# Performance work log

Hardware: AMD Instinct MI355X
Metric: run time of the kernel (lower is better)

## Reference

```python
import jax, jax.numpy as jnp
import numpy as np

B, S, H = 2, 2048, 2048
NH, NKV, HD = 16, 4, 128
NEG = -1e9


def rotate_half(x):
    x1, x2 = x[..., : x.shape[-1] // 2], x[..., x.shape[-1] // 2 :]
    return jnp.concatenate((-x2, x1), axis=-1)


def setup_inputs() -> dict:
    key = jax.random.key(0)
    ks = jax.random.split(key, 6)
    hidden_states = jax.random.normal(ks[0], (B, S, H), dtype=jnp.float32)
    # causal additive mask [B, 1, S, S]
    causal = jnp.tril(jnp.ones((S, S), dtype=bool))
    attention_mask = jnp.where(causal, 0.0, NEG).astype(jnp.float32)
    attention_mask = jnp.broadcast_to(attention_mask, (B, 1, S, S))
    # rotary embeddings, base 10000
    inv_freq = 1.0 / (10000.0 ** (np.arange(0, HD, 2, dtype=np.float32) / HD))
    pos = np.arange(S, dtype=np.float32)
    freqs = np.outer(pos, inv_freq)  # [S, HD/2]
    emb = np.concatenate([freqs, freqs], axis=-1)  # [S, HD]
    cos = jnp.broadcast_to(jnp.asarray(np.cos(emb)), (B, S, HD))
    sin = jnp.broadcast_to(jnp.asarray(np.sin(emb)), (B, S, HD))
    sc = 0.02
    Wq = jax.random.normal(ks[1], (H, NH * HD), dtype=jnp.float32) * sc
    Wk = jax.random.normal(ks[2], (H, NKV * HD), dtype=jnp.float32) * sc
    Wv = jax.random.normal(ks[3], (H, NKV * HD), dtype=jnp.float32) * sc
    Wo = jax.random.normal(ks[4], (H, H), dtype=jnp.float32) * sc
    return {"hidden_states": hidden_states, "attention_mask": attention_mask,
            "cos": cos, "sin": sin, "Wq": Wq, "Wk": Wk, "Wv": Wv, "Wo": Wo}


def reference(hidden_states, attention_mask, cos, sin, Wq, Wk, Wv, Wo):
    b, s, _ = hidden_states.shape
    # projections -> [b, heads, s, hd]
    q = (hidden_states @ Wq).reshape(b, s, NH, HD).transpose(0, 2, 1, 3)
    k = (hidden_states @ Wk).reshape(b, s, NKV, HD).transpose(0, 2, 1, 3)
    v = (hidden_states @ Wv).reshape(b, s, NKV, HD).transpose(0, 2, 1, 3)
    # RoPE (cos/sin unsqueezed at dim 1)
    c, sn = cos[:, None], sin[:, None]
    q = q * c + rotate_half(q) * sn
    k = k * c + rotate_half(k) * sn
    # GQA repeat_kv: [b, nkv, s, hd] -> [b, nh, s, hd]
    n_rep = NH // NKV
    k = jnp.repeat(k, n_rep, axis=1)
    v = jnp.repeat(v, n_rep, axis=1)
    scores = jnp.einsum("bhqd,bhkd->bhqk", q, k) / jnp.sqrt(jnp.float32(HD))
    scores = scores + attention_mask
    probs = jax.nn.softmax(scores.astype(jnp.float32), axis=-1).astype(q.dtype)
    out = jnp.einsum("bhqk,bhkd->bhqd", probs, v)
    out = out.transpose(0, 2, 1, 3).reshape(b, s, NH * HD)
    return out @ Wo
```

## Files before the change

kernel.cpp:

```cpp
#include <hip/hip_runtime.h>
#include <hip/hip_bf16.h>

typedef __bf16 bf16;
typedef __bf16 bf16x4 __attribute__((ext_vector_type(4)));
typedef __bf16 bf16x8 __attribute__((ext_vector_type(8)));
typedef float f32x4 __attribute__((ext_vector_type(4)));

__device__ __forceinline__ void gload_lds16(const void* g, void* l) {
  __builtin_amdgcn_global_load_lds((__attribute__((address_space(1))) void*)(g),
                                   (__attribute__((address_space(3))) void*)(l), 16, 0, 0);
}
__device__ __forceinline__ float fexp2(float x) {
  float r;
  asm volatile("v_exp_f32 %0, %1" : "=v"(r) : "v"(x));
  return r;
}
#define S_WAITCNT_VM(n) asm volatile("s_waitcnt vmcnt(" #n ")" ::: "memory")

__global__ void k_diag(float* __restrict__ o, float v) { o[threadIdx.x] = v; }

__global__ void k_cvt_bf16(const float* __restrict__ x, bf16* __restrict__ y, int n4) {
  int i = blockIdx.x * blockDim.x + threadIdx.x;
  if (i < n4) {
    float4 v = reinterpret_cast<const float4*>(x)[i];
    bf16x4 o = {(bf16)v.x, (bf16)v.y, (bf16)v.z, (bf16)v.w};
    reinterpret_cast<bf16x4*>(y)[i] = o;
  }
}

__global__ void k_transpose_w(const float* __restrict__ W, bf16* __restrict__ Wt, int K, int N) {
  __shared__ float tile[32][33];
  int kb = blockIdx.x * 32, nb = blockIdx.y * 32;
  int tx = threadIdx.x & 31, ty = threadIdx.x >> 5;
#pragma unroll
  for (int i = 0; i < 32; i += 8)
    tile[ty + i][tx] = W[(size_t)(kb + ty + i) * N + nb + tx];
  __syncthreads();
#pragma unroll
  for (int i = 0; i < 32; i += 8)
    Wt[(size_t)(nb + ty + i) * K + kb + tx] = (bf16)tile[tx][ty + i];
}

__global__ void k_transpose_v(const bf16* __restrict__ Cq, bf16* __restrict__ Vt) {
  __shared__ bf16 tile[32][34];
  constexpr int S = 2048, CSTR = 3072;
  int sb = blockIdx.x * 32, db = blockIdx.y * 32, bh = blockIdx.z;
  int b = bh >> 2, kvh = bh & 3;
  int tx = threadIdx.x & 31, ty = threadIdx.x >> 5;
  const bf16* src = Cq + (size_t)b * S * CSTR + 2560 + kvh * 128;
#pragma unroll
  for (int i = 0; i < 32; i += 8)
    tile[ty + i][tx] = src[(size_t)(sb + ty + i) * CSTR + db + tx];
  __syncthreads();
  bf16* dst = Vt + (size_t)bh * 128 * S;
#pragma unroll
  for (int i = 0; i < 32; i += 8)
    dst[(size_t)(db + ty + i) * S + sb + tx] = tile[tx][ty + i];
}

template <typename OT>
__global__ __launch_bounds__(512) void k_gemm3(const bf16* __restrict__ A,
                                               const bf16* __restrict__ B0,
                                               const bf16* __restrict__ B1, int nsplit,
                                               OT* __restrict__ C, int Ncols, int Kd) {
  __shared__ __align__(16) bf16 lds_[65536];
  char* lds = (char*)lds_;
  const int t = threadIdx.x, w = t >> 6, l = t & 63;
  const int lr = l & 15, lk = l >> 4;
  const int gx = gridDim.x;
  const int flat = blockIdx.y * gx + blockIdx.x;
  const int xcd = flat & 7, local = flat >> 3;
  const int mi = (xcd & 3) * (gx >> 2) + (local & ((gx >> 2) - 1));
  const int ni = (xcd >> 2) * (gridDim.y >> 1) + (local >> 2);
  const int m0 = mi * 256, n0 = ni * 256;
  const int wm = w >> 2, wn = w & 3;
  const bf16* Bt = (n0 < nsplit) ? B0 + (size_t)n0 * Kd : B1 + (size_t)(n0 - nsplit) * Kd;
  const int nkt = Kd >> 6;
  const int srow = l >> 2;
  const int lch = (l & 3) ^ ((srow + (srow >> 2)) & 3);
  auto stA = [&](int tile, int unit) {
    if (tile >= nkt) return;
    const bf16* s = A + (size_t)(m0 + unit * 64 + (w >> 1) * 16 + srow) * Kd +
                    (tile << 6) + (w & 1) * 32 + lch * 8;
    gload_lds16(s, lds + (tile & 1) * 32768 + unit * 8192 + w * 1024);
  };
  auto stB = [&](int tile, int grp) {
    if (tile >= nkt) return;
    const bf16* s = Bt + (size_t)((w >> 1) * 64 + grp * 16 + srow) * Kd +
                    (tile << 6) + (w & 1) * 32 + lch * 8;
    gload_lds16(s, lds + 65536 + (tile & 1) * 32768 + grp * 8192 + w * 1024);
  };
  const int rdoff = lr * 64 + ((lk ^ ((lr + (lr >> 2)) & 3)) << 4);

  f32x4 acc[8][4] = {};
  stA(0, 0); stA(0, 1); stA(0, 2); stA(0, 3);
  stB(0, 0);
  stA(1, 0); stB(0, 1); stA(1, 1); stB(0, 2); stA(1, 2); stB(0, 3);

  for (int kt = 0; kt < nkt; ++kt) {
    const int buf = kt & 1;
    const char* Ab = lds + buf * 32768;
    const char* Bb = lds + 65536 + buf * 32768;
    bf16x8 af[8][2];
#pragma unroll
    for (int p = 0; p < 4; ++p) {
      if (kt + 1 < nkt) { S_WAITCNT_VM(6); } else { S_WAITCNT_VM(0); }
      __builtin_amdgcn_sched_barrier(0);
      __builtin_amdgcn_s_barrier();
      __builtin_amdgcn_sched_barrier(0);
      if (p == 0) stA(kt + 1, 3); else stA(kt + 2, p - 1);
      stB(kt + 1, p);
      if (p == 0) {
#pragma unroll
        for (int i = 0; i < 8; ++i) {
          const char* ub = Ab + (wm * 2 + (i >> 2)) * 8192 + (i & 3) * 2048;
          af[i][0] = *reinterpret_cast<const bf16x8*>(ub + rdoff);
          af[i][1] = *reinterpret_cast<const bf16x8*>(ub + 1024 + rdoff);
        }
      }
      bf16x8 b0 = *reinterpret_cast<const bf16x8*>(Bb + p * 8192 + wn * 2048 + rdoff);
      bf16x8 b1 = *reinterpret_cast<const bf16x8*>(Bb + p * 8192 + wn * 2048 + 1024 + rdoff);
      __builtin_amdgcn_s_setprio(1);
#pragma unroll
      for (int i = 0; i < 8; ++i) {
        acc[i][p] = __builtin_amdgcn_mfma_f32_16x16x32_bf16(af[i][0], b0, acc[i][p], 0, 0, 0);
        acc[i][p] = __builtin_amdgcn_mfma_f32_16x16x32_bf16(af[i][1], b1, acc[i][p], 0, 0, 0);
      }
      __builtin_amdgcn_s_setprio(0);
      __builtin_amdgcn_sched_barrier(0);
    }
  }
#pragma unroll
  for (int i = 0; i < 8; ++i)
#pragma unroll
    for (int j = 0; j < 4; ++j)
#pragma unroll
      for (int r = 0; r < 4; ++r) {
        int row = m0 + wm * 128 + i * 16 + lk * 4 + r;
        int col = n0 + wn * 64 + j * 16 + lr;
        if constexpr (sizeof(OT) == 4)
          C[(size_t)row * Ncols + col] = acc[i][j][r];
        else
          C[(size_t)row * Ncols + col] = (bf16)acc[i][j][r];
      }
}

template <int BM, typename OT>
__global__ __launch_bounds__(512) void k_gemm2(const bf16* __restrict__ A, const bf16* __restrict__ Bt,
                                               OT* __restrict__ C, int N, int Kd) {
  constexpr int NA = (BM / 16) * 2;
  constexpr int NB = 16;
  constexpr int NST = NA + NB;
  constexpr int NSW = NST / 8;
  constexpr int WM = BM / 4;
  constexpr int RG = WM / 16;
  __shared__ __align__(16) bf16 sAB[2][NST * 512];
  const int t = threadIdx.x, w = t >> 6, l = t & 63;
  const int lr = l & 15, lk = l >> 4;
  const int gx = gridDim.x;
  const int nwg = gx * gridDim.y;
  const int flat = blockIdx.y * gx + blockIdx.x;
  const int vid = (flat & 7) * (nwg >> 3) + (flat >> 3);
  const int m0 = (vid % gx) * BM, n0 = (vid / gx) * 128;
  const int wm = w >> 1, wn = w & 1;
  const int srow = l >> 2;
  const int lchunk = (l & 3) ^ (((l >> 5) & 1) << 1);
  const int rdoff = lr * 64 + ((lk * 16) ^ ((lr >> 3) << 5));
  const int nkt = Kd >> 6;
  char* lds = (char*)sAB;

  auto stage = [&](int kt, int buf) {
    const int k0 = kt << 6;
#pragma unroll
    for (int u = 0; u < NSW; ++u) {
      const int s = w * NSW + u;
      const bf16* src;
      if (s < NA)
        src = A + (size_t)(m0 + (s >> 1) * 16 + srow) * Kd + k0 + (s & 1) * 32 + lchunk * 8;
      else
        src = Bt + (size_t)(n0 + ((s - NA) >> 1) * 16 + srow) * Kd + k0 + ((s - NA) & 1) * 32 + lchunk * 8;
      gload_lds16(src, lds + buf * (NST * 1024) + s * 1024);
    }
  };

  f32x4 acc[RG][4] = {};
  stage(0, 0);
  stage(1, 1);
  if constexpr (NSW == 6) S_WAITCNT_VM(6); else S_WAITCNT_VM(4);
  __builtin_amdgcn_s_barrier();
  int c = 0;
  for (int kt = 0; kt < nkt; ++kt) {
    __builtin_amdgcn_sched_barrier(0);
    const char* base = lds + c * (NST * 1024);
    bf16x8 af[RG][2], bfr[4][2];
#pragma unroll
    for (int i = 0; i < RG; ++i)
#pragma unroll
      for (int kk = 0; kk < 2; ++kk)
        af[i][kk] = *reinterpret_cast<const bf16x8*>(base + ((wm * RG + i) * 2 + kk) * 1024 + rdoff);
#pragma unroll
    for (int j = 0; j < 4; ++j)
#pragma unroll
      for (int kk = 0; kk < 2; ++kk)
        bfr[j][kk] = *reinterpret_cast<const bf16x8*>(base + (NA + (wn * 4 + j) * 2 + kk) * 1024 + rdoff);
    __builtin_amdgcn_s_setprio(1);
#pragma unroll
    for (int i = 0; i < RG; ++i)
#pragma unroll
      for (int j = 0; j < 4; ++j) {
        acc[i][j] = __builtin_amdgcn_mfma_f32_16x16x32_bf16(af[i][0], bfr[j][0], acc[i][j], 0, 0, 0);
        acc[i][j] = __builtin_amdgcn_mfma_f32_16x16x32_bf16(af[i][1], bfr[j][1], acc[i][j], 0, 0, 0);
      }
    __builtin_amdgcn_s_setprio(0);
    __builtin_amdgcn_sched_barrier(0);
    asm volatile("" ::: "memory");
    __builtin_amdgcn_s_barrier();
    if (kt + 2 < nkt) stage(kt + 2, c);
    if (kt + 1 < nkt) {
      if (kt + 2 < nkt) {
        if constexpr (NSW == 6) S_WAITCNT_VM(6); else S_WAITCNT_VM(4);
      } else {
        S_WAITCNT_VM(0);
      }
      asm volatile("" ::: "memory");
      __builtin_amdgcn_s_barrier();
    }
    c ^= 1;
  }
#pragma unroll
  for (int i = 0; i < RG; ++i)
#pragma unroll
    for (int j = 0; j < 4; ++j)
#pragma unroll
      for (int r = 0; r < 4; ++r) {
        int row = m0 + wm * WM + i * 16 + lk * 4 + r;
        int col = n0 + wn * 64 + j * 16 + lr;
        if constexpr (sizeof(OT) == 4)
          C[(size_t)row * N + col] = acc[i][j][r];
        else
          C[(size_t)row * N + col] = (bf16)acc[i][j][r];
      }
}

__global__ void k_rope(bf16* __restrict__ X, const float* __restrict__ cs, const float* __restrict__ sn,
                       int nh, int rowstride, float scale, int total) {
  int idx = blockIdx.x * blockDim.x + threadIdx.x;
  if (idx >= total) return;
  int d = idx & 63;
  int th = idx >> 6;
  int h = th % nh;
  int tok = th / nh;
  size_t base = (size_t)tok * rowstride + h * 128;
  float c = cs[tok * 128 + d], s = sn[tok * 128 + d];
  float x1 = (float)X[base + d];
  float x2 = (float)X[base + d + 64];
  X[base + d] = (bf16)((x1 * c - x2 * s) * scale);
  X[base + d + 64] = (bf16)((x2 * c + x1 * s) * scale);
}

__global__ __launch_bounds__(256) void k_attn(const bf16* __restrict__ Q, const bf16* __restrict__ KV,
                                              const bf16* __restrict__ Vt, bf16* __restrict__ O) {
  constexpr int S = 2048, HD = 128, QSTR = 3072, OSTR = 2048;
  __shared__ __align__(16) bf16 sK[2][64 * 128];
  __shared__ __align__(16) bf16 sV[2][128 * 64];
  __shared__ __align__(16) bf16 sP[4][16][72];
  const int bid = blockIdx.x;
  const int vid = (bid & 7) * 32 + (bid >> 3);
  const int p = vid & 7, bh = vid >> 3;
  const int h = bh & 15, b = bh >> 4;
  const int t = threadIdx.x, w = t >> 6, l = t & 63;
  const int lr = l & 15, lk = l >> 4;
  const int kvh = h >> 2;
  const int swz = (lr & 7) << 4;

  const char* kbase = (const char*)(KV + (size_t)b * S * QSTR + kvh * HD);
  const int krow_l = w * 16 + (l >> 4);
  const int kcol_l = (l & 15) << 4;
  const char* vtbase = (const char*)(Vt + (size_t)(b * 4 + kvh) * HD * S);
  const int vrow_l = w * 32 + (l >> 3);
  const int vcol_l = (l & 7) << 4;
  char* sKb = (char*)sK;
  char* sVb = (char*)sV;
  auto stage = [&](int kvb, int buf) {
#pragma unroll
    for (int c = 0; c < 4; ++c) {
      const int krow = krow_l + c * 4;
      gload_lds16(kbase + (size_t)(kvb + krow) * (QSTR * 2) + (kcol_l ^ ((krow & 7) << 4)),
                  sKb + buf * 16384 + (w * 4 + c) * 1024);
      const int vrow = vrow_l + c * 8;
      gload_lds16(vtbase + (size_t)vrow * (S * 2) + kvb * 2 + (vcol_l ^ ((vrow & 7) << 4)),
                  sVb + buf * 16384 + (w * 4 + c) * 1024);
    }
  };

  for (int seg = 0; seg < 2; ++seg) {
    const int qtl = seg ? (15 - p) : p;
    const int qw = qtl * 128 + w * 32;
    const int qlast = qw + 31;
    const int ntiles = (qtl + 1) * 2;
    int cur = 0;
    __syncthreads();
    stage(0, 0);
    bf16x8 qf[2][4];
#pragma unroll
    for (int rg = 0; rg < 2; ++rg) {
      const bf16* Qp = Q + (size_t)(b * S + qw + rg * 16 + lr) * QSTR + h * HD + lk * 8;
#pragma unroll
      for (int i = 0; i < 4; ++i) qf[rg][i] = *reinterpret_cast<const bf16x8*>(Qp + i * 32);
    }
    f32x4 oacc[2][8] = {};
    float mrow[2][4] = {{-3e38f, -3e38f, -3e38f, -3e38f}, {-3e38f, -3e38f, -3e38f, -3e38f}};
    float lsum[2][4] = {};
    __syncthreads();
    for (int tt = 0; tt < ntiles; ++tt) {
      const int kvb = tt * 64;
      if (tt + 1 < ntiles) stage(kvb + 64, cur ^ 1);
      const char* sKc = sKb + cur * 16384;
      const char* sVc = sVb + cur * 16384;
      if (kvb <= qlast) {
        float pm[2][4][4];
#pragma unroll
        for (int c = 0; c < 4; ++c) {
          f32x4 s0 = {}, s1 = {};
#pragma unroll
          for (int kf = 0; kf < 4; ++kf) {
            bf16x8 kf8 = *reinterpret_cast<const bf16x8*>(
                sKc + (c * 16 + lr) * 256 + (((kf * 64) + (lk << 4)) ^ swz));
            s0 = __builtin_amdgcn_mfma_f32_16x16x32_bf16(qf[0][kf], kf8, s0, 0, 0, 0);
            s1 = __builtin_amdgcn_mfma_f32_16x16x32_bf16(qf[1][kf], kf8, s1, 0, 0, 0);
          }
#pragma unroll
          for (int r = 0; r < 4; ++r) { pm[0][c][r] = s0[r]; pm[1][c][r] = s1[r]; }
        }
        if (kvb + 63 > qw) {
#pragma unroll
          for (int rg = 0; rg < 2; ++rg)
#pragma unroll
            for (int c = 0; c < 4; ++c) {
              const int col = kvb + c * 16 + lr;
#pragma unroll
              for (int r = 0; r < 4; ++r)
                if (col > qw + rg * 16 + lk * 4 + r) pm[rg][c][r] = -3e38f;
            }
        }
        float pmax[2][4];
#pragma unroll
        for (int rg = 0; rg < 2; ++rg)
#pragma unroll
          for (int r = 0; r < 4; ++r)
            pmax[rg][r] = fmaxf(fmaxf(pm[rg][0][r], pm[rg][1][r]), fmaxf(pm[rg][2][r], pm[rg][3][r]));
        bool hi = false;
#pragma unroll
        for (int rg = 0; rg < 2; ++rg)
#pragma unroll
          for (int r = 0; r < 4; ++r) hi |= (pmax[rg][r] > mrow[rg][r] + 8.f);
        if (__any(hi)) {
          float mx[2][4];
#pragma unroll
          for (int rg = 0; rg < 2; ++rg)
#pragma unroll
            for (int r = 0; r < 4; ++r) mx[rg][r] = pmax[rg][r];
#pragma unroll
          for (int off = 1; off < 16; off <<= 1)
#pragma unroll
            for (int rg = 0; rg < 2; ++rg)
#pragma unroll
              for (int r = 0; r < 4; ++r) mx[rg][r] = fmaxf(mx[rg][r], __shfl_xor(mx[rg][r], off));
#pragma unroll
          for (int rg = 0; rg < 2; ++rg)
#pragma unroll
            for (int r = 0; r < 4; ++r) {
              float mn = fmaxf(mrow[rg][r], mx[rg][r]);
              float fac = fexp2(mrow[rg][r] - mn);
              mrow[rg][r] = mn;
              lsum[rg][r] *= fac;
#pragma unroll
              for (int ch = 0; ch < 8; ++ch) oacc[rg][ch][r] *= fac;
            }
        }
#pragma unroll
        for (int rg = 0; rg < 2; ++rg) {
#pragma unroll
          for (int c = 0; c < 4; ++c)
#pragma unroll
            for (int r = 0; r < 4; ++r) pm[rg][c][r] = fexp2(pm[rg][c][r] - mrow[rg][r]);
#pragma unroll
          for (int r = 0; r < 4; ++r)
            lsum[rg][r] += (pm[rg][0][r] + pm[rg][1][r]) + (pm[rg][2][r] + pm[rg][3][r]);
        }
        bf16x8 pf[2][2];
#pragma unroll
        for (int rg = 0; rg < 2; ++rg) {
#pragma unroll
          for (int c = 0; c < 4; ++c)
#pragma unroll
            for (int r = 0; r < 4; ++r) sP[w][lk * 4 + r][c * 16 + lr] = (bf16)pm[rg][c][r];
          pf[rg][0] = *reinterpret_cast<const bf16x8*>(&sP[w][lr][lk * 8]);
          pf[rg][1] = *reinterpret_cast<const bf16x8*>(&sP[w][lr][32 + lk * 8]);
        }
#pragma unroll
        for (int ch = 0; ch < 8; ++ch) {
          bf16x8 vf0 = *reinterpret_cast<const bf16x8*>(
              sVc + (ch * 16 + lr) * 128 + ((lk << 4) ^ swz));
          bf16x8 vf1 = *reinterpret_cast<const bf16x8*>(
              sVc + (ch * 16 + lr) * 128 + ((64 + (lk << 4)) ^ swz));
          oacc[0][ch] = __builtin_amdgcn_mfma_f32_16x16x32_bf16(pf[0][0], vf0, oacc[0][ch], 0, 0, 0);
          oacc[0][ch] = __builtin_amdgcn_mfma_f32_16x16x32_bf16(pf[0][1], vf1, oacc[0][ch], 0, 0, 0);
          oacc[1][ch] = __builtin_amdgcn_mfma_f32_16x16x32_bf16(pf[1][0], vf0, oacc[1][ch], 0, 0, 0);
          oacc[1][ch] = __builtin_amdgcn_mfma_f32_16x16x32_bf16(pf[1][1], vf1, oacc[1][ch], 0, 0, 0);
        }
      }
      __syncthreads();
      cur ^= 1;
    }
#pragma unroll
    for (int off = 1; off < 16; off <<= 1)
#pragma unroll
      for (int rg = 0; rg < 2; ++rg)
#pragma unroll
        for (int r = 0; r < 4; ++r) lsum[rg][r] += __shfl_xor(lsum[rg][r], off);
#pragma unroll
    for (int rg = 0; rg < 2; ++rg) {
      float inv[4];
#pragma unroll
      for (int r = 0; r < 4; ++r) inv[r] = 1.0f / lsum[rg][r];
      bf16* Op = O + (size_t)(b * S + qw + rg * 16) * OSTR + h * HD;
#pragma unroll
      for (int ch = 0; ch < 8; ++ch)
#pragma unroll
        for (int r = 0; r < 4; ++r)
          Op[(size_t)(lk * 4 + r) * OSTR + ch * 16 + lr] = (bf16)(oacc[rg][ch][r] * inv[r]);
    }
  }
}

extern "C" void kernel_launch(void* const* d_in, const int* in_sizes, int n_in,
                              void* d_out, int out_size, void* d_ws, size_t ws_size,
                              hipStream_t stream) {
  const float* hs = (const float*)d_in[0];
  const float* cosb = (const float*)d_in[2];
  const float* sinb = (const float*)d_in[3];
  const float* Wq = (const float*)d_in[4];
  const float* Wk = (const float*)d_in[5];
  const float* Wv = (const float*)d_in[6];
  const float* Wo = (const float*)d_in[7];
  float* out = (float*)d_out;

  constexpr int B = 2, S = 2048, H = 2048, NH = 16, NKV = 4, HD = 128;
  constexpr int T = B * S;
  constexpr size_t MB = 1024 * 1024;

  const size_t ws_need = 24 * MB;
  if (ws_size < ws_need) {
    k_diag<<<1, 64, 0, stream>>>(out, 1000.0f + (float)(ws_size / MB));
    return;
  }
  bf16* Xb = (bf16*)d_ws;
  bf16* WtQ = (bf16*)((char*)d_ws + 16 * MB);
  bf16* Ob = Xb;
  bf16* Cqkv = (bf16*)d_out;
  bf16* Vtb = (bf16*)((char*)d_out + 24 * MB);
  bf16* WtKV = (bf16*)((char*)d_out + 28 * MB);

  k_cvt_bf16<<<T * H / 4 / 256, 256, 0, stream>>>(hs, Xb, T * H / 4);

  k_transpose_w<<<dim3(H / 32, H / 32), 256, 0, stream>>>(Wq, WtQ, H, H);
  k_transpose_w<<<dim3(H / 32, (NKV * HD) / 32), 256, 0, stream>>>(Wk, WtKV, H, NKV * HD);
  k_transpose_w<<<dim3(H / 32, (NKV * HD) / 32), 256, 0, stream>>>(Wv, WtKV + (size_t)(NKV * HD) * H, H, NKV * HD);

  k_gemm3<bf16><<<dim3(16, 12), 512, 0, stream>>>(Xb, WtQ, WtKV, 2048, Cqkv, 3072, H);

  k_transpose_v<<<dim3(S / 32, HD / 32, B * NKV), 256, 0, stream>>>(Cqkv, Vtb);

  const float qscale = 0.12751743f;
  k_rope<<<(T * NH * 64) / 256, 256, 0, stream>>>(Cqkv, cosb, sinb, NH, 3072, qscale, T * NH * 64);
  k_rope<<<(T * NKV * 64) / 256, 256, 0, stream>>>(Cqkv + 2048, cosb, sinb, NKV, 3072, 1.0f, T * NKV * 64);

  k_attn<<<256, 256, 0, stream>>>(Cqkv, Cqkv + 2048, Vtb, Ob);

  k_transpose_w<<<dim3(H / 32, H / 32), 256, 0, stream>>>(Wo, WtQ, H, H);
  k_gemm2<256, float><<<dim3(16, 16), 512, 0, stream>>>(Ob, WtQ, out, H, H);
}
```

Before: 234.2 us.

## Split each KV tile across two wave groups in attention and merge partial softmax

The attention kernel now launches 512 threads per block. Each of the four query waves is paired with a second wave, and the two process different 32-column halves of every 64-key tile. At the end of each segment, the second wave group writes its partial output, running max and sum to shared memory. The first group then merges them with a rescaled log-sum-exp combine before storing. The aim is more waves per CU to hide latency with the same 256-block grid. The cost is a larger shared-memory footprint, an extra merge step with a block-wide sync, and fewer MFMAs per wave per tile.

Measured after the change: 224.9 us. 1.04x faster.

```diff
diff --git a/kernel.cpp b/kernel.cpp
--- a/kernel.cpp
+++ b/kernel.cpp
@@ -258,44 +258,42 @@
   X[base + d + 64] = (bf16)((x2 * c + x1 * s) * scale);
 }
 
-__global__ __launch_bounds__(256) void k_attn(const bf16* __restrict__ Q, const bf16* __restrict__ KV,
+__global__ __launch_bounds__(512) void k_attn(const bf16* __restrict__ Q, const bf16* __restrict__ KV,
                                               const bf16* __restrict__ Vt, bf16* __restrict__ O) {
   constexpr int S = 2048, HD = 128, QSTR = 3072, OSTR = 2048;
-  __shared__ __align__(16) bf16 sK[2][64 * 128];
-  __shared__ __align__(16) bf16 sV[2][128 * 64];
-  __shared__ __align__(16) bf16 sP[4][16][72];
+  __shared__ __align__(16) char smem[81920];
   const int bid = blockIdx.x;
   const int vid = (bid & 7) * 32 + (bid >> 3);
   const int p = vid & 7, bh = vid >> 3;
   const int h = bh & 15, b = bh >> 4;
   const int t = threadIdx.x, w = t >> 6, l = t & 63;
+  const int wq = w & 3, wk = w >> 2;
   const int lr = l & 15, lk = l >> 4;
   const int kvh = h >> 2;
   const int swz = (lr & 7) << 4;
 
   const char* kbase = (const char*)(KV + (size_t)b * S * QSTR + kvh * HD);
-  const int krow_l = w * 16 + (l >> 4);
+  const int krow_l = w * 8 + (l >> 4);
   const int kcol_l = (l & 15) << 4;
   const char* vtbase = (const char*)(Vt + (size_t)(b * 4 + kvh) * HD * S);
-  const int vrow_l = w * 32 + (l >> 3);
+  const int vrow_l = w * 16 + (l >> 3);
   const int vcol_l = (l & 7) << 4;
-  char* sKb = (char*)sK;
-  char* sVb = (char*)sV;
   auto stage = [&](int kvb, int buf) {
 #pragma unroll
-    for (int c = 0; c < 4; ++c) {
+    for (int c = 0; c < 2; ++c) {
       const int krow = krow_l + c * 4;
       gload_lds16(kbase + (size_t)(kvb + krow) * (QSTR * 2) + (kcol_l ^ ((krow & 7) << 4)),
-                  sKb + buf * 16384 + (w * 4 + c) * 1024);
+                  smem + buf * 16384 + (w * 2 + c) * 1024);
       const int vrow = vrow_l + c * 8;
       gload_lds16(vtbase + (size_t)vrow * (S * 2) + kvb * 2 + (vcol_l ^ ((vrow & 7) << 4)),
-                  sVb + buf * 16384 + (w * 4 + c) * 1024);
+                  smem + 32768 + buf * 16384 + (w * 2 + c) * 1024);
     }
   };
+  char* sPb = smem + 65536 + w * 1280;
 
   for (int seg = 0; seg < 2; ++seg) {
     const int qtl = seg ? (15 - p) : p;
-    const int qw = qtl * 128 + w * 32;
+    const int qw = qtl * 128 + wq * 32;
     const int qlast = qw + 31;
     const int ntiles = (qtl + 1) * 2;
     int cur = 0;
@@ -309,46 +307,46 @@
       for (int i = 0; i < 4; ++i) qf[rg][i] = *reinterpret_cast<const bf16x8*>(Qp + i * 32);
     }
     f32x4 oacc[2][8] = {};
-    float mrow[2][4] = {{-3e38f, -3e38f, -3e38f, -3e38f}, {-3e38f, -3e38f, -3e38f, -3e38f}};
+    float mrow[2][4] = {{-1e30f, -1e30f, -1e30f, -1e30f}, {-1e30f, -1e30f, -1e30f, -1e30f}};
     float lsum[2][4] = {};
     __syncthreads();
     for (int tt = 0; tt < ntiles; ++tt) {
       const int kvb = tt * 64;
       if (tt + 1 < ntiles) stage(kvb + 64, cur ^ 1);
-      const char* sKc = sKb + cur * 16384;
-      const char* sVc = sVb + cur * 16384;
-      if (kvb <= qlast) {
-        float pm[2][4][4];
-#pragma unroll
-        for (int c = 0; c < 4; ++c) {
+      const char* sKc = smem + cur * 16384;
+      const char* sVc = smem + 32768 + cur * 16384;
+      const int col0 = kvb + wk * 32;
+      if (col0 <= qlast) {
+        float pm[2][2][4];
+#pragma unroll
+        for (int c = 0; c < 2; ++c) {
           f32x4 s0 = {}, s1 = {};
 #pragma unroll
           for (int kf = 0; kf < 4; ++kf) {
             bf16x8 kf8 = *reinterpret_cast<const bf16x8*>(
-                sKc + (c * 16 + lr) * 256 + (((kf * 64) + (lk << 4)) ^ swz));
+                sKc + (wk * 32 + c * 16 + lr) * 256 + (((kf * 64) + (lk << 4)) ^ swz));
             s0 = __builtin_amdgcn_mfma_f32_16x16x32_bf16(qf[0][kf], kf8, s0, 0, 0, 0);
             s1 = __builtin_amdgcn_mfma_f32_16x16x32_bf16(qf[1][kf], kf8, s1, 0, 0, 0);
           }
 #pragma unroll
           for (int r = 0; r < 4; ++r) { pm[0][c][r] = s0[r]; pm[1][c][r] = s1[r]; }
         }
-        if (kvb + 63 > qw) {
+        if (col0 + 31 > qw) {
 #pragma unroll
           for (int rg = 0; rg < 2; ++rg)
 #pragma unroll
-            for (int c = 0; c < 4; ++c) {
-              const int col = kvb + c * 16 + lr;
+            for (int c = 0; c < 2; ++c) {
+              const int col = col0 + c * 16 + lr;
 #pragma unroll
               for (int r = 0; r < 4; ++r)
-                if (col > qw + rg * 16 + lk * 4 + r) pm[rg][c][r] = -3e38f;
+                if (col > qw + rg * 16 + lk * 4 + r) pm[rg][c][r] = -1e38f;
             }
         }
         float pmax[2][4];
 #pragma unroll
         for (int rg = 0; rg < 2; ++rg)
 #pragma unroll
-          for (int r = 0; r < 4; ++r)
-            pmax[rg][r] = fmaxf(fmaxf(pm[rg][0][r], pm[rg][1][r]), fmaxf(pm[rg][2][r], pm[rg][3][r]));
+          for (int r = 0; r < 4; ++r) pmax[rg][r] = fmaxf(pm[rg][0][r], pm[rg][1][r]);
         bool hi = false;
 #pragma unroll
         for (int rg = 0; rg < 2; ++rg)
@@ -381,33 +379,28 @@
 #pragma unroll
         for (int rg = 0; rg < 2; ++rg) {
 #pragma unroll
-          for (int c = 0; c < 4; ++c)
+          for (int c = 0; c < 2; ++c)
 #pragma unroll
             for (int r = 0; r < 4; ++r) pm[rg][c][r] = fexp2(pm[rg][c][r] - mrow[rg][r]);
 #pragma unroll
-          for (int r = 0; r < 4; ++r)
-            lsum[rg][r] += (pm[rg][0][r] + pm[rg][1][r]) + (pm[rg][2][r] + pm[rg][3][r]);
-        }
-        bf16x8 pf[2][2];
+          for (int r = 0; r < 4; ++r) lsum[rg][r] += pm[rg][0][r] + pm[rg][1][r];
+        }
+        bf16x8 pf[2];
 #pragma unroll
         for (int rg = 0; rg < 2; ++rg) {
 #pragma unroll
-          for (int c = 0; c < 4; ++c)
-#pragma unroll
-            for (int r = 0; r < 4; ++r) sP[w][lk * 4 + r][c * 16 + lr] = (bf16)pm[rg][c][r];
-          pf[rg][0] = *reinterpret_cast<const bf16x8*>(&sP[w][lr][lk * 8]);
-          pf[rg][1] = *reinterpret_cast<const bf16x8*>(&sP[w][lr][32 + lk * 8]);
+          for (int c = 0; c < 2; ++c)
+#pragma unroll
+            for (int r = 0; r < 4; ++r)
+              *(bf16*)(sPb + (lk * 4 + r) * 80 + (c * 16 + lr) * 2) = (bf16)pm[rg][c][r];
+          pf[rg] = *reinterpret_cast<const bf16x8*>(sPb + lr * 80 + lk * 16);
         }
 #pragma unroll
         for (int ch = 0; ch < 8; ++ch) {
-          bf16x8 vf0 = *reinterpret_cast<const bf16x8*>(
-              sVc + (ch * 16 + lr) * 128 + ((lk << 4) ^ swz));
-          bf16x8 vf1 = *reinterpret_cast<const bf16x8*>(
-              sVc + (ch * 16 + lr) * 128 + ((64 + (lk << 4)) ^ swz));
-          oacc[0][ch] = __builtin_amdgcn_mfma_f32_16x16x32_bf16(pf[0][0], vf0, oacc[0][ch], 0, 0, 0);
-          oacc[0][ch] = __builtin_amdgcn_mfma_f32_16x16x32_bf16(pf[0][1], vf1, oacc[0][ch], 0, 0, 0);
-          oacc[1][ch] = __builtin_amdgcn_mfma_f32_16x16x32_bf16(pf[1][0], vf0, oacc[1][ch], 0, 0, 0);
-          oacc[1][ch] = __builtin_amdgcn_mfma_f32_16x16x32_bf16(pf[1][1], vf1, oacc[1][ch], 0, 0, 0);
+          bf16x8 vf = *reinterpret_cast<const bf16x8*>(
+              sVc + (ch * 16 + lr) * 128 + ((wk * 64 + (lk << 4)) ^ swz));
+          oacc[0][ch] = __builtin_amdgcn_mfma_f32_16x16x32_bf16(pf[0], vf, oacc[0][ch], 0, 0, 0);
+          oacc[1][ch] = __builtin_amdgcn_mfma_f32_16x16x32_bf16(pf[1], vf, oacc[1][ch], 0, 0, 0);
         }
       }
       __syncthreads();
@@ -419,17 +412,48 @@
       for (int rg = 0; rg < 2; ++rg)
 #pragma unroll
         for (int r = 0; r < 4; ++r) lsum[rg][r] += __shfl_xor(lsum[rg][r], off);
-#pragma unroll
-    for (int rg = 0; rg < 2; ++rg) {
-      float inv[4];
-#pragma unroll
-      for (int r = 0; r < 4; ++r) inv[r] = 1.0f / lsum[rg][r];
-      bf16* Op = O + (size_t)(b * S + qw + rg * 16) * OSTR + h * HD;
-#pragma unroll
-      for (int ch = 0; ch < 8; ++ch)
-#pragma unroll
-        for (int r = 0; r < 4; ++r)
-          Op[(size_t)(lk * 4 + r) * OSTR + ch * 16 + lr] = (bf16)(oacc[rg][ch][r] * inv[r]);
+    float* ob = (float*)smem;
+    float* mlb = (float*)(smem + 65536);
+    if (wk == 1) {
+#pragma unroll
+      for (int rg = 0; rg < 2; ++rg) {
+#pragma unroll
+        for (int ch = 0; ch < 8; ++ch)
+          *reinterpret_cast<f32x4*>(&ob[wq * 4096 + l * 64 + (rg * 8 + ch) * 4]) = oacc[rg][ch];
+#pragma unroll
+        for (int r = 0; r < 4; ++r) {
+          mlb[wq * 1024 + l * 16 + rg * 8 + r] = mrow[rg][r];
+          mlb[wq * 1024 + l * 16 + rg * 8 + 4 + r] = lsum[rg][r];
+        }
+      }
+    }
+    __syncthreads();
+    if (wk == 0) {
+      float sc0[2][4], sc1[2][4];
+#pragma unroll
+      for (int rg = 0; rg < 2; ++rg)
+#pragma unroll
+        for (int r = 0; r < 4; ++r) {
+          float m1 = mlb[wq * 1024 + l * 16 + rg * 8 + r];
+          float l1 = mlb[wq * 1024 + l * 16 + rg * 8 + 4 + r];
+          float m = fmaxf(mrow[rg][r], m1);
+          float w0 = fexp2(mrow[rg][r] - m), w1 = fexp2(m1 - m);
+          float inv = 1.0f / (lsum[rg][r] * w0 + l1 * w1);
+          sc0[rg][r] = w0 * inv;
+          sc1[rg][r] = w1 * inv;
+        }
+#pragma unroll
+      for (int rg = 0; rg < 2; ++rg) {
+        bf16* Op = O + (size_t)(b * S + qw + rg * 16) * OSTR + h * HD;
+#pragma unroll
+        for (int ch = 0; ch < 8; ++ch) {
+          f32x4 o1 = *reinterpret_cast<const f32x4*>(&ob[wq * 4096 + l * 64 + (rg * 8 + ch) * 4]);
+#pragma unroll
+          for (int r = 0; r < 4; ++r)
+            Op[(size_t)(lk * 4 + r) * OSTR + ch * 16 + lr] =
+                (bf16)(oacc[rg][ch][r] * sc0[rg][r] + o1[r] * sc1[rg][r]);
+        }
+      }
     }
   }
 }
@@ -476,7 +500,7 @@
   k_rope<<<(T * NH * 64) / 256, 256, 0, stream>>>(Cqkv, cosb, sinb, NH, 3072, qscale, T * NH * 64);
   k_rope<<<(T * NKV * 64) / 256, 256, 0, stream>>>(Cqkv + 2048, cosb, sinb, NKV, 3072, 1.0f, T * NKV * 64);
 
-  k_attn<<<256, 256, 0, stream>>>(Cqkv, Cqkv + 2048, Vtb, Ob);
+  k_attn<<<256, 512, 0, stream>>>(Cqkv, Cqkv + 2048, Vtb, Ob);
 
   k_transpose_w<<<dim3(H / 32, H / 32), 256, 0, stream>>>(Wo, WtQ, H, H);
   k_gemm2<256, float><<<dim3(16, 16), 512, 0, stream>>>(Ob, WtQ, out, H, H);
```
